# Optimization experiments

Measured on AMD Instinct MI355X. Metric: run time of the kernel, lower is better.

Reference implementation:

```python
import jax, jax.numpy as jnp
import numpy as np

B, S, E = 2, 2048, 1024
H, D = 16, 64          # num_heads, head_dim
FF = 4096              # ff_dim = 4*E
EPS = 1e-5


def _layer_norm(x, g, b):
    mu = jnp.mean(x, axis=-1, keepdims=True)
    var = jnp.mean(jnp.square(x - mu), axis=-1, keepdims=True)
    return (x - mu) * jax.lax.rsqrt(var + EPS) * g + b


def setup_inputs() -> dict:
    key = jax.random.key(0)
    ks = jax.random.split(key, 9)
    s = lambda fan_in: 1.0 / np.sqrt(fan_in)
    return {
        "x": jax.random.normal(ks[0], (B, S, E), dtype=jnp.float32),
        "w_qkv": jax.random.uniform(ks[1], (3 * E, E), jnp.float32, -s(E), s(E)),
        "b_qkv": jnp.zeros((3 * E,), jnp.float32),
        "w_out": jax.random.uniform(ks[2], (E, E), jnp.float32, -s(E), s(E)),
        "b_out": jnp.zeros((E,), jnp.float32),
        "g1": jnp.ones((E,), jnp.float32),
        "beta1": jnp.zeros((E,), jnp.float32),
        "w_fc1": jax.random.uniform(ks[3], (FF, E), jnp.float32, -s(E), s(E)),
        "b_fc1": jnp.zeros((FF,), jnp.float32),
        "w_fc2": jax.random.uniform(ks[4], (E, FF), jnp.float32, -s(FF), s(FF)),
        "b_fc2": jnp.zeros((E,), jnp.float32),
        "g2": jnp.ones((E,), jnp.float32),
        "beta2": jnp.zeros((E,), jnp.float32),
    }


def reference(x, w_qkv, b_qkv, w_out, b_out, g1, beta1, w_fc1, b_fc1, w_fc2, b_fc2, g2, beta2):
    scale = 1.0 / np.sqrt(D)
    # QKV projection: [B,S,3E] -> [3,B,H,S,D]
    qkv = (x @ w_qkv.T + b_qkv).reshape(B, S, 3, H, D).transpose(2, 0, 3, 1, 4)
    q, k, v = qkv[0], qkv[1], qkv[2]
    attn = jax.nn.softmax(jnp.einsum('bhqd,bhkd->bhqk', q, k) * scale, axis=-1)
    out = jnp.einsum('bhqk,bhkd->bhqd', attn, v)          # [B,H,S,D]
    out = out.transpose(0, 2, 1, 3).reshape(B, S, E)
    attn_out = out @ w_out.T + b_out
    x1 = _layer_norm(x + attn_out, g1, beta1)
    h = jax.nn.gelu(x1 @ w_fc1.T + b_fc1, approximate=False)  # torch GELU = exact erf
    ff_out = h @ w_fc2.T + b_fc2
    return _layer_norm(x1 + ff_out, g2, beta2)
```

## Files before the change

### kernel.cpp

```cpp
#include <hip/hip_runtime.h>
#include <hip/hip_bf16.h>
#include <math.h>
#include <type_traits>

typedef __hip_bfloat16 bf16;
using short8  = __attribute__((ext_vector_type(8))) short;
using short4v = __attribute__((ext_vector_type(4))) short;
using f32x4   = __attribute__((ext_vector_type(4))) float;

#define TS 2048
#define TH 16
#define TD 64
#define TE 1024
#define T3E 3072

__device__ __forceinline__ void gload16(void* lds, const void* g) {
    __builtin_amdgcn_global_load_lds(
        (__attribute__((address_space(1))) void*)g,
        (__attribute__((address_space(3))) void*)lds, 16, 0, 0);
}

__device__ __forceinline__ uint32_t pkbf16(float a, float b) {
    return (uint32_t)__bfloat16_as_ushort(__float2bfloat16(a)) |
           ((uint32_t)__bfloat16_as_ushort(__float2bfloat16(b)) << 16);
}

__global__ __launch_bounds__(256) void f2b_multi(
    const float* __restrict__ s0, bf16* __restrict__ d0,
    const float* __restrict__ s1, bf16* __restrict__ d1,
    const float* __restrict__ s2, bf16* __restrict__ d2,
    const float* __restrict__ s3, bf16* __restrict__ d3,
    const float* __restrict__ s4, bf16* __restrict__ d4)
{
    int blk = blockIdx.x;
    const float* s; bf16* d; int base;
    if (blk < 2048)      { s = s0; d = d0; base = 0; }
    else if (blk < 3584) { s = s1; d = d1; base = 2048; }
    else if (blk < 4096) { s = s2; d = d2; base = 3584; }
    else if (blk < 6144) { s = s3; d = d3; base = 4096; }
    else                 { s = s4; d = d4; base = 6144; }
    size_t i = ((size_t)(blk - base) * 256 + threadIdx.x) * 8;
    float4 a = *(const float4*)&s[i];
    float4 b = *(const float4*)&s[i + 4];
    bf16 t[8];
    t[0] = __float2bfloat16(a.x); t[1] = __float2bfloat16(a.y);
    t[2] = __float2bfloat16(a.z); t[3] = __float2bfloat16(a.w);
    t[4] = __float2bfloat16(b.x); t[5] = __float2bfloat16(b.y);
    t[6] = __float2bfloat16(b.z); t[7] = __float2bfloat16(b.w);
    *(uint4*)&d[i] = *(uint4*)t;
}

template <typename TC, bool GELU, bool QS>
__global__ __launch_bounds__(256) void gemm_bt(
    const bf16* __restrict__ A, const bf16* __restrict__ Bw,
    const float* __restrict__ bias, TC* __restrict__ C,
    int M, int N, int K, int kLen)
{
    __shared__ bf16 As[128 * 32];
    __shared__ bf16 Bs[128 * 32];

    const int t    = threadIdx.x;
    const int lane = t & 63;
    const int wave = t >> 6;
    const int wr   = wave >> 1;
    const int wc   = wave & 1;
    const int lr   = lane & 15;
    const int lq   = lane >> 4;
    const int mBase = blockIdx.y * 128;
    const int nBase = blockIdx.x * 128;
    const int kOff  = blockIdx.z * kLen;

    const int srow = lane >> 2;
    const int skc  = (lane & 3) * 8;

    f32x4 acc[4][4];
    #pragma unroll
    for (int mi = 0; mi < 4; mi++)
        #pragma unroll
        for (int ni = 0; ni < 4; ni++)
            acc[mi][ni] = (f32x4){0.f, 0.f, 0.f, 0.f};

    for (int k0 = kOff; k0 < kOff + kLen; k0 += 32) {
        #pragma unroll
        for (int c = 0; c < 2; c++) {
            int r0 = wave * 32 + c * 16;
            gload16(&As[r0 * 32],
                    &A[(size_t)(mBase + r0 + srow) * K + k0 + skc]);
            gload16(&Bs[r0 * 32],
                    &Bw[(size_t)(nBase + r0 + srow) * K + k0 + skc]);
        }
        __syncthreads();

        short8 af[4], bfr[4];
        #pragma unroll
        for (int mi = 0; mi < 4; mi++)
            af[mi] = *(const short8*)&As[(wr * 64 + mi * 16 + lr) * 32 + lq * 8];
        #pragma unroll
        for (int ni = 0; ni < 4; ni++)
            bfr[ni] = *(const short8*)&Bs[(wc * 64 + ni * 16 + lr) * 32 + lq * 8];

        #pragma unroll
        for (int mi = 0; mi < 4; mi++)
            #pragma unroll
            for (int ni = 0; ni < 4; ni++)
                acc[mi][ni] = __builtin_amdgcn_mfma_f32_16x16x32_bf16(
                    af[mi], bfr[ni], acc[mi][ni], 0, 0, 0);
        __syncthreads();
    }

    const size_t cOff = (size_t)blockIdx.z * M * N;
    #pragma unroll
    for (int mi = 0; mi < 4; mi++) {
        #pragma unroll
        for (int ni = 0; ni < 4; ni++) {
            int c = nBase + wc * 64 + ni * 16 + lr;
            float bv = (blockIdx.z == 0) ? bias[c] : 0.f;
            #pragma unroll
            for (int i = 0; i < 4; i++) {
                int r = mBase + wr * 64 + mi * 16 + lq * 4 + i;
                float v = acc[mi][ni][i] + bv;
                if constexpr (GELU)
                    v = 0.5f * v * (1.0f + erff(v * 0.70710678118f));
                if constexpr (QS)
                    if (c < TE) v *= 0.180336880111f;
                if constexpr (std::is_same_v<TC, bf16>)
                    C[cOff + (size_t)r * N + c] = __float2bfloat16(v);
                else
                    C[cOff + (size_t)r * N + c] = v;
            }
        }
    }
}

__global__ __launch_bounds__(256) void vtrans(
    const bf16* __restrict__ qkv, bf16* __restrict__ vT)
{
    __shared__ bf16 T[64 * 72];
    const int t  = threadIdx.x;
    const int s0 = blockIdx.x * 64;
    const int bh = blockIdx.y;
    const int b = bh >> 4, h = bh & 15;
    const size_t srcBase = ((size_t)b * TS + s0) * T3E + 2 * TE + h * TD;

    #pragma unroll
    for (int i = 0; i < 2; i++) {
        int tok = (t >> 3) + i * 32;
        int c   = t & 7;
        int cw  = c ^ ((tok >> 3) & 7);
        *(uint4*)&T[tok * 72 + cw * 8] =
            *(const uint4*)&qkv[srcBase + (size_t)tok * T3E + c * 8];
    }
    __syncthreads();
    #pragma unroll
    for (int i = 0; i < 2; i++) {
        int d   = (t >> 3) + i * 32;
        int sof = (t & 7) * 8;
        bf16 tmp[8];
        #pragma unroll
        for (int j = 0; j < 8; j++) {
            int s = sof + j;
            tmp[j] = T[s * 72 + (((d >> 3) ^ ((s >> 3) & 7)) << 3) + (d & 7)];
        }
        *(uint4*)&vT[((size_t)bh * TD + d) * TS + s0 + sof] = *(uint4*)tmp;
    }
}

__global__ __launch_bounds__(256, 4) void attn_flash(
    const bf16* __restrict__ qkv, const bf16* __restrict__ vT,
    bf16* __restrict__ attnO)
{
    __shared__ bf16 Ks[128 * 72];
    __shared__ bf16 Vt[64 * 136];

    const int t    = threadIdx.x;
    const int lane = t & 63;
    const int wv   = t >> 6;
    const int c    = lane & 15;
    const int u    = lane >> 4;
    const int qt   = blockIdx.x;
    const int bh   = blockIdx.y;
    const int h = bh & 15, b = bh >> 4;
    const size_t tokBase = (size_t)b * TS;
    const int qrow = qt * 64 + wv * 16 + c;

    short8 qf[2];
    #pragma unroll
    for (int kc = 0; kc < 2; kc++)
        qf[kc] = *(const short8*)&qkv[(tokBase + qrow) * T3E + h * TD + kc * 32 + u * 8];

    f32x4 oacc[4];
    #pragma unroll
    for (int di = 0; di < 4; di++) oacc[di] = (f32x4){0.f, 0.f, 0.f, 0.f};
    float lsum = 0.f;

    const int vd = t >> 2;
    const int vc = (t & 3) * 8;

    for (int it = 0; it < 16; it++) {
        const int kb0 = it * 128;
        __syncthreads();

        #pragma unroll
        for (int i = 0; i < 4; i++) {
            int l = t + i * 256;
            int r = l >> 3, ch = (l & 7) * 8;
            *(uint4*)&Ks[r * 72 + ch] =
                *(const uint4*)&qkv[(tokBase + kb0 + r) * T3E + TE + h * TD + ch];
        }
        {
            const bf16* vs = &vT[((size_t)bh * TD + vd) * TS + kb0 + vc];
            #pragma unroll
            for (int i = 0; i < 4; i++)
                *(uint4*)&Vt[vd * 136 + vc + i * 32] = *(const uint4*)&vs[i * 32];
        }
        __syncthreads();

        f32x4 sacc[8];
        #pragma unroll
        for (int kc = 0; kc < 2; kc++) {
            #pragma unroll
            for (int kb = 0; kb < 8; kb++) {
                short8 kf = *(const short8*)&Ks[(kb * 16 + c) * 72 + kc * 32 + u * 8];
                sacc[kb] = __builtin_amdgcn_mfma_f32_16x16x32_bf16(
                    kf, qf[kc],
                    kc == 0 ? (f32x4){0.f, 0.f, 0.f, 0.f} : sacc[kb], 0, 0, 0);
            }
        }

        uint32_t pT[8][2];
        #pragma unroll
        for (int kb = 0; kb < 8; kb++) {
            float p0 = exp2f(fminf(sacc[kb][0], 80.f));
            float p1 = exp2f(fminf(sacc[kb][1], 80.f));
            float p2 = exp2f(fminf(sacc[kb][2], 80.f));
            float p3 = exp2f(fminf(sacc[kb][3], 80.f));
            lsum += (p0 + p1) + (p2 + p3);
            pT[kb][0] = pkbf16(p0, p1);
            pT[kb][1] = pkbf16(p2, p3);
        }

        #pragma unroll
        for (int kb = 0; kb < 8; kb++) {
            union { uint32_t d[2]; short4v s; } pb;
            pb.d[0] = pT[kb][0];
            pb.d[1] = pT[kb][1];
            #pragma unroll
            for (int di = 0; di < 4; di++) {
                short4v va = *(const short4v*)&Vt[(di * 16 + c) * 136 + kb * 16 + u * 4];
                oacc[di] = __builtin_amdgcn_mfma_f32_16x16x16bf16_1k(
                    va, pb.s, oacc[di], 0, 0, 0);
            }
        }
    }

    lsum += __shfl_xor(lsum, 16, 64);
    lsum += __shfl_xor(lsum, 32, 64);
    const float inv = 1.0f / lsum;

    #pragma unroll
    for (int di = 0; di < 4; di++) {
        bf16 ob[4];
        #pragma unroll
        for (int rg = 0; rg < 4; rg++)
            ob[rg] = __float2bfloat16(oacc[di][rg] * inv);
        *(uint2*)&attnO[(tokBase + qrow) * TE + h * TD + di * 16 + u * 4] = *(uint2*)ob;
    }
}

__global__ __launch_bounds__(256) void add_ln3(
    const float* __restrict__ a, const float* __restrict__ p0,
    const float* __restrict__ p1, const float* __restrict__ g,
    const float* __restrict__ beta, float* __restrict__ out,
    bf16* __restrict__ outb)
{
    __shared__ float r1[256], r2[256];
    const int t = threadIdx.x;
    const size_t row = (size_t)blockIdx.x * TE;

    float4 va = *(const float4*)&a[row + t * 4];
    float4 v0 = *(const float4*)&p0[row + t * 4];
    float4 v1 = *(const float4*)&p1[row + t * 4];
    float v[4] = {va.x + v0.x + v1.x, va.y + v0.y + v1.y,
                  va.z + v0.z + v1.z, va.w + v0.w + v1.w};
    float s = 0.f, s2 = 0.f;
    #pragma unroll
    for (int i = 0; i < 4; i++) { s += v[i]; s2 += v[i] * v[i]; }
    r1[t] = s; r2[t] = s2;
    __syncthreads();
    for (int off = 128; off > 0; off >>= 1) {
        if (t < off) { r1[t] += r1[t + off]; r2[t] += r2[t + off]; }
        __syncthreads();
    }
    const float mu  = r1[0] * (1.f / 1024.f);
    const float var = r2[0] * (1.f / 1024.f) - mu * mu;
    const float rs  = rsqrtf(var + 1e-5f);
    float4 vg  = *(const float4*)&g[t * 4];
    float4 vbt = *(const float4*)&beta[t * 4];
    float o[4];
    o[0] = (v[0] - mu) * rs * vg.x + vbt.x;
    o[1] = (v[1] - mu) * rs * vg.y + vbt.y;
    o[2] = (v[2] - mu) * rs * vg.z + vbt.z;
    o[3] = (v[3] - mu) * rs * vg.w + vbt.w;
    *(float4*)&out[row + t * 4] = *(float4*)o;
    if (outb) {
        bf16 ob[4];
        #pragma unroll
        for (int i = 0; i < 4; i++) ob[i] = __float2bfloat16(o[i]);
        *(uint2*)&outb[row + t * 4] = *(uint2*)ob;
    }
}

extern "C" void kernel_launch(void* const* d_in, const int* in_sizes, int n_in,
                              void* d_out, int out_size, void* d_ws, size_t ws_size,
                              hipStream_t stream)
{
    const float* x     = (const float*)d_in[0];
    const float* w_qkv = (const float*)d_in[1];
    const float* b_qkv = (const float*)d_in[2];
    const float* w_out = (const float*)d_in[3];
    const float* b_out = (const float*)d_in[4];
    const float* g1    = (const float*)d_in[5];
    const float* beta1 = (const float*)d_in[6];
    const float* w_fc1 = (const float*)d_in[7];
    const float* b_fc1 = (const float*)d_in[8];
    const float* w_fc2 = (const float*)d_in[9];
    const float* b_fc2 = (const float*)d_in[10];
    const float* g2    = (const float*)d_in[11];
    const float* beta2 = (const float*)d_in[12];
    float* out = (float*)d_out;

    char* wsb   = (char*)d_ws;
    bf16*  qkv   = (bf16*)(wsb);
    bf16*  hbuf  = (bf16*)(wsb);
    bf16*  attnO = (bf16*)(wsb + 33554432);
    float* y     = (float*)(wsb + 41943040);
    float* ff    = y;
    bf16*  xb    = (bf16*)(wsb + 75497472);
    bf16*  vT    = (bf16*)(wsb + 75497472);
    float* x1    = (float*)(wsb + 75497472);
    bf16*  x1b   = (bf16*)(wsb + 92274688);
    bf16*  wqkvb = (bf16*)(wsb + 100663296);
    bf16*  woutb = (bf16*)(wsb + 106954752);
    bf16*  wfc1b = (bf16*)(wsb + 109051904);
    bf16*  wfc2b = (bf16*)(wsb + 117440512);

    const int M = 2 * TS;
    const size_t PART = (size_t)M * TE;
    dim3 blk(256);

    f2b_multi<<<dim3(8192), blk, 0, stream>>>(
        x, xb, w_qkv, wqkvb, w_out, woutb, w_fc1, wfc1b, w_fc2, wfc2b);

    gemm_bt<bf16, false, true><<<dim3(24, 32, 1), blk, 0, stream>>>(
        xb, wqkvb, b_qkv, qkv, M, T3E, TE, TE);
    vtrans<<<dim3(TS / 64, 2 * TH), blk, 0, stream>>>(qkv, vT);
    attn_flash<<<dim3(TS / 64, 2 * TH), blk, 0, stream>>>(qkv, vT, attnO);
    gemm_bt<float, false, false><<<dim3(8, 32, 2), blk, 0, stream>>>(
        attnO, woutb, b_out, y, M, TE, TE, TE / 2);
    add_ln3<<<dim3(M), blk, 0, stream>>>(x, y, y + PART, g1, beta1, x1, x1b);
    gemm_bt<bf16, true, false><<<dim3(32, 32, 1), blk, 0, stream>>>(
        x1b, wfc1b, b_fc1, hbuf, M, 4096, TE, TE);
    gemm_bt<float, false, false><<<dim3(8, 32, 2), blk, 0, stream>>>(
        hbuf, wfc2b, b_fc2, ff, M, TE, 4096, 2048);
    add_ln3<<<dim3(M), blk, 0, stream>>>(x1, ff, ff + PART, g2, beta2, out, nullptr);
}
```

Before: 427.9 us.

## Fuse V transpose into QKV GEMM epilogue and prefetch K/V tiles in attention

The QKV GEMM epilogue now writes the V columns straight into a transposed, permuted vT buffer, which removes the separate vtrans kernel and its extra pass over V. The attention kernel keeps the next K/V tile in registers while the current tile is being used, remaps block indices so heads are interleaved, and reads V with 8-wide LDS loads feeding two MFMAs, with the key order permuted to match the new vT layout. This adds register pressure in the attention kernel and scattered 8-byte stores in the GEMM epilogue, and the vT buffer is moved to another workspace region.

```diff
diff --git a/kernel.cpp b/kernel.cpp
--- a/kernel.cpp
+++ b/kernel.cpp
@@ -50,11 +50,11 @@
     *(uint4*)&d[i] = *(uint4*)t;
 }
 
-template <typename TC, bool GELU, bool QS>
+template <typename TC, bool GELU, bool QS, bool WVT>
 __global__ __launch_bounds__(256) void gemm_bt(
     const bf16* __restrict__ A, const bf16* __restrict__ Bw,
     const float* __restrict__ bias, TC* __restrict__ C,
-    int M, int N, int K, int kLen)
+    bf16* __restrict__ vTout, int M, int N, int K, int kLen)
 {
     __shared__ bf16 As[128 * 32];
     __shared__ bf16 Bs[128 * 32];
@@ -113,55 +113,41 @@
     for (int mi = 0; mi < 4; mi++) {
         #pragma unroll
         for (int ni = 0; ni < 4; ni++) {
-            int c = nBase + wc * 64 + ni * 16 + lr;
-            float bv = (blockIdx.z == 0) ? bias[c] : 0.f;
-            #pragma unroll
-            for (int i = 0; i < 4; i++) {
-                int r = mBase + wr * 64 + mi * 16 + lq * 4 + i;
-                float v = acc[mi][ni][i] + bv;
-                if constexpr (GELU)
-                    v = 0.5f * v * (1.0f + erff(v * 0.70710678118f));
-                if constexpr (QS)
-                    if (c < TE) v *= 0.180336880111f;
-                if constexpr (std::is_same_v<TC, bf16>)
-                    C[cOff + (size_t)r * N + c] = __float2bfloat16(v);
-                else
-                    C[cOff + (size_t)r * N + c] = v;
-            }
-        }
-    }
-}
-
-__global__ __launch_bounds__(256) void vtrans(
-    const bf16* __restrict__ qkv, bf16* __restrict__ vT)
-{
-    __shared__ bf16 T[64 * 72];
-    const int t  = threadIdx.x;
-    const int s0 = blockIdx.x * 64;
-    const int bh = blockIdx.y;
-    const int b = bh >> 4, h = bh & 15;
-    const size_t srcBase = ((size_t)b * TS + s0) * T3E + 2 * TE + h * TD;
-
-    #pragma unroll
-    for (int i = 0; i < 2; i++) {
-        int tok = (t >> 3) + i * 32;
-        int c   = t & 7;
-        int cw  = c ^ ((tok >> 3) & 7);
-        *(uint4*)&T[tok * 72 + cw * 8] =
-            *(const uint4*)&qkv[srcBase + (size_t)tok * T3E + c * 8];
-    }
-    __syncthreads();
-    #pragma unroll
-    for (int i = 0; i < 2; i++) {
-        int d   = (t >> 3) + i * 32;
-        int sof = (t & 7) * 8;
-        bf16 tmp[8];
-        #pragma unroll
-        for (int j = 0; j < 8; j++) {
-            int s = sof + j;
-            tmp[j] = T[s * 72 + (((d >> 3) ^ ((s >> 3) & 7)) << 3) + (d & 7)];
-        }
-        *(uint4*)&vT[((size_t)bh * TD + d) * TS + s0 + sof] = *(uint4*)tmp;
+            int cc = nBase + wc * 64 + ni * 16 + lr;
+            float bv = (blockIdx.z == 0) ? bias[cc] : 0.f;
+            int r0 = mBase + wr * 64 + mi * 16 + lq * 4;
+            bool vpath = false;
+            if constexpr (WVT) {
+                if (cc >= 2 * TE) {
+                    vpath = true;
+                    int d  = cc - 2 * TE;
+                    int s0 = r0 & (TS - 1);
+                    int bb = r0 >> 11;
+                    int pos = (s0 & ~31) | (((s0 >> 2) & 3) << 3)
+                            | (((s0 >> 4) & 1) << 2);
+                    bf16 ob[4];
+                    #pragma unroll
+                    for (int i = 0; i < 4; i++)
+                        ob[i] = __float2bfloat16(acc[mi][ni][i] + bv);
+                    *(uint2*)&vTout[((size_t)(bb * TH + (d >> 6)) * TD + (d & 63))
+                                    * TS + pos] = *(uint2*)ob;
+                }
+            }
+            if (!vpath) {
+                #pragma unroll
+                for (int i = 0; i < 4; i++) {
+                    float v = acc[mi][ni][i] + bv;
+                    if constexpr (GELU)
+                        v = 0.5f * v * (1.0f + erff(v * 0.70710678118f));
+                    if constexpr (QS)
+                        if (cc < TE) v *= 0.180336880111f;
+                    if constexpr (std::is_same_v<TC, bf16>)
+                        C[cOff + (size_t)(r0 + i) * N + cc] = __float2bfloat16(v);
+                    else
+                        C[cOff + (size_t)(r0 + i) * N + cc] = v;
+                }
+            }
+        }
     }
 }
 
@@ -177,8 +163,9 @@
     const int wv   = t >> 6;
     const int c    = lane & 15;
     const int u    = lane >> 4;
-    const int qt   = blockIdx.x;
-    const int bh   = blockIdx.y;
+    const int bid  = blockIdx.x;
+    const int bh   = (bid & 7) * 4 + ((bid >> 3) & 3);
+    const int qt   = bid >> 5;
     const int h = bh & 15, b = bh >> 4;
     const size_t tokBase = (size_t)b * TS;
     const int qrow = qt * 64 + wv * 16 + c;
@@ -193,27 +180,44 @@
     for (int di = 0; di < 4; di++) oacc[di] = (f32x4){0.f, 0.f, 0.f, 0.f};
     float lsum = 0.f;
 
-    const int vd = t >> 2;
-    const int vc = (t & 3) * 8;
+    const int kr  = t >> 3;
+    const int kc8 = (t & 7) * 8;
+    const int vd  = t >> 2;
+    const int vc  = (t & 3) * 8;
+
+    uint4 kreg[4], vreg[4];
+    const bf16* vbase = &vT[((size_t)bh * TD + vd) * TS + vc];
+
+    {
+        #pragma unroll
+        for (int i = 0; i < 4; i++)
+            kreg[i] = *(const uint4*)&qkv[(tokBase + kr + i * 32) * T3E + TE + h * TD + kc8];
+        #pragma unroll
+        for (int i = 0; i < 4; i++)
+            vreg[i] = *(const uint4*)&vbase[i * 32];
+    }
 
     for (int it = 0; it < 16; it++) {
-        const int kb0 = it * 128;
-        __syncthreads();
-
-        #pragma unroll
-        for (int i = 0; i < 4; i++) {
-            int l = t + i * 256;
-            int r = l >> 3, ch = (l & 7) * 8;
-            *(uint4*)&Ks[r * 72 + ch] =
-                *(const uint4*)&qkv[(tokBase + kb0 + r) * T3E + TE + h * TD + ch];
-        }
-        {
-            const bf16* vs = &vT[((size_t)bh * TD + vd) * TS + kb0 + vc];
+        __syncthreads();
+
+        #pragma unroll
+        for (int i = 0; i < 4; i++)
+            *(uint4*)&Ks[(kr + i * 32) * 72 + kc8] = kreg[i];
+        #pragma unroll
+        for (int i = 0; i < 4; i++)
+            *(uint4*)&Vt[vd * 136 + vc + i * 32] = vreg[i];
+        __syncthreads();
+
+        if (it < 15) {
+            const int kb1 = (it + 1) * 128;
             #pragma unroll
             for (int i = 0; i < 4; i++)
-                *(uint4*)&Vt[vd * 136 + vc + i * 32] = *(const uint4*)&vs[i * 32];
-        }
-        __syncthreads();
+                kreg[i] = *(const uint4*)&qkv[(tokBase + kb1 + kr + i * 32) * T3E
+                                              + TE + h * TD + kc8];
+            #pragma unroll
+            for (int i = 0; i < 4; i++)
+                vreg[i] = *(const uint4*)&vbase[kb1 + i * 32];
+        }
 
         f32x4 sacc[8];
         #pragma unroll
@@ -227,28 +231,31 @@
             }
         }
 
-        uint32_t pT[8][2];
-        #pragma unroll
-        for (int kb = 0; kb < 8; kb++) {
-            float p0 = exp2f(fminf(sacc[kb][0], 80.f));
-            float p1 = exp2f(fminf(sacc[kb][1], 80.f));
-            float p2 = exp2f(fminf(sacc[kb][2], 80.f));
-            float p3 = exp2f(fminf(sacc[kb][3], 80.f));
-            lsum += (p0 + p1) + (p2 + p3);
-            pT[kb][0] = pkbf16(p0, p1);
-            pT[kb][1] = pkbf16(p2, p3);
-        }
-
-        #pragma unroll
-        for (int kb = 0; kb < 8; kb++) {
-            union { uint32_t d[2]; short4v s; } pb;
-            pb.d[0] = pT[kb][0];
-            pb.d[1] = pT[kb][1];
+        #pragma unroll
+        for (int p = 0; p < 4; p++) {
+            union { uint32_t d[2]; short4v s; } pb0, pb1;
+            {
+                float a0 = exp2f(fminf(sacc[2*p][0], 80.f));
+                float a1 = exp2f(fminf(sacc[2*p][1], 80.f));
+                float a2 = exp2f(fminf(sacc[2*p][2], 80.f));
+                float a3 = exp2f(fminf(sacc[2*p][3], 80.f));
+                float b0 = exp2f(fminf(sacc[2*p+1][0], 80.f));
+                float b1 = exp2f(fminf(sacc[2*p+1][1], 80.f));
+                float b2 = exp2f(fminf(sacc[2*p+1][2], 80.f));
+                float b3 = exp2f(fminf(sacc[2*p+1][3], 80.f));
+                lsum += (a0 + a1) + (a2 + a3) + (b0 + b1) + (b2 + b3);
+                pb0.d[0] = pkbf16(a0, a1); pb0.d[1] = pkbf16(a2, a3);
+                pb1.d[0] = pkbf16(b0, b1); pb1.d[1] = pkbf16(b2, b3);
+            }
             #pragma unroll
             for (int di = 0; di < 4; di++) {
-                short4v va = *(const short4v*)&Vt[(di * 16 + c) * 136 + kb * 16 + u * 4];
+                short8 vv = *(const short8*)&Vt[(di * 16 + c) * 136 + p * 32 + u * 8];
+                short4v lo = __builtin_shufflevector(vv, vv, 0, 1, 2, 3);
+                short4v hi = __builtin_shufflevector(vv, vv, 4, 5, 6, 7);
                 oacc[di] = __builtin_amdgcn_mfma_f32_16x16x16bf16_1k(
-                    va, pb.s, oacc[di], 0, 0, 0);
+                    lo, pb0.s, oacc[di], 0, 0, 0);
+                oacc[di] = __builtin_amdgcn_mfma_f32_16x16x16bf16_1k(
+                    hi, pb1.s, oacc[di], 0, 0, 0);
             }
         }
     }
@@ -333,10 +340,10 @@
     bf16*  qkv   = (bf16*)(wsb);
     bf16*  hbuf  = (bf16*)(wsb);
     bf16*  attnO = (bf16*)(wsb + 33554432);
+    bf16*  vT    = (bf16*)(wsb + 41943040);
     float* y     = (float*)(wsb + 41943040);
     float* ff    = y;
     bf16*  xb    = (bf16*)(wsb + 75497472);
-    bf16*  vT    = (bf16*)(wsb + 75497472);
     float* x1    = (float*)(wsb + 75497472);
     bf16*  x1b   = (bf16*)(wsb + 92274688);
     bf16*  wqkvb = (bf16*)(wsb + 100663296);
@@ -351,16 +358,15 @@
     f2b_multi<<<dim3(8192), blk, 0, stream>>>(
         x, xb, w_qkv, wqkvb, w_out, woutb, w_fc1, wfc1b, w_fc2, wfc2b);
 
-    gemm_bt<bf16, false, true><<<dim3(24, 32, 1), blk, 0, stream>>>(
-        xb, wqkvb, b_qkv, qkv, M, T3E, TE, TE);
-    vtrans<<<dim3(TS / 64, 2 * TH), blk, 0, stream>>>(qkv, vT);
-    attn_flash<<<dim3(TS / 64, 2 * TH), blk, 0, stream>>>(qkv, vT, attnO);
-    gemm_bt<float, false, false><<<dim3(8, 32, 2), blk, 0, stream>>>(
-        attnO, woutb, b_out, y, M, TE, TE, TE / 2);
+    gemm_bt<bf16, false, true, true><<<dim3(24, 32, 1), blk, 0, stream>>>(
+        xb, wqkvb, b_qkv, qkv, vT, M, T3E, TE, TE);
+    attn_flash<<<dim3(1024), blk, 0, stream>>>(qkv, vT, attnO);
+    gemm_bt<float, false, false, false><<<dim3(8, 32, 2), blk, 0, stream>>>(
+        attnO, woutb, b_out, y, nullptr, M, TE, TE, TE / 2);
     add_ln3<<<dim3(M), blk, 0, stream>>>(x, y, y + PART, g1, beta1, x1, x1b);
-    gemm_bt<bf16, true, false><<<dim3(32, 32, 1), blk, 0, stream>>>(
-        x1b, wfc1b, b_fc1, hbuf, M, 4096, TE, TE);
-    gemm_bt<float, false, false><<<dim3(8, 32, 2), blk, 0, stream>>>(
-        hbuf, wfc2b, b_fc2, ff, M, TE, 4096, 2048);
+    gemm_bt<bf16, true, false, false><<<dim3(32, 32, 1), blk, 0, stream>>>(
+        x1b, wfc1b, b_fc1, hbuf, nullptr, M, 4096, TE, TE);
+    gemm_bt<float, false, false, false><<<dim3(8, 32, 2), blk, 0, stream>>>(
+        hbuf, wfc2b, b_fc2, ff, nullptr, M, TE, 4096, 2048);
     add_ln3<<<dim3(M), blk, 0, stream>>>(x1, ff, ff + PART, g2, beta2, out, nullptr);
 }
```

Result: slower. 510.1 us (+19.2%).
